# Optimization experiments

Measured on AMD Instinct MI355X. Metric: run time of the kernel, lower is better.

The kernel has to match this reference:

```python
import jax, jax.numpy as jnp
import numpy as np

BN_EPS = 1e-5
CLAMP = 1e-10


def _three_nn(q, p):
    # q: (B,N,3) query points, p: (B,M,3) reference points
    # returns dist (B,N,3) euclidean distance to 3 nearest, idx (B,N,3)
    d2 = (jnp.sum(q * q, -1)[:, :, None] + jnp.sum(p * p, -1)[:, None, :]
          - 2.0 * jnp.einsum('bnd,bmd->bnm', q, p))  # (B,N,M)
    neg_vals, idx = jax.lax.top_k(-d2, 3)
    dist = jnp.sqrt(jnp.maximum(-neg_vals, 1e-20))
    return dist, idx


def _gather(feats_t, idx):
    # feats_t: (B,M,C), idx: (B,N,3) -> (B,N,3,C)
    return jax.vmap(lambda f, i: f[i])(feats_t, idx)


def _conv_bn_relu(x, W, b, g, beta):
    # x: (B,Cin,N); 1x1 Conv1d + BatchNorm1d (training-mode batch stats) + relu
    y = jnp.einsum('oc,bcn->bon', W, x) + b[None, :, None]
    mean = jnp.mean(y, axis=(0, 2), keepdims=True)
    var = jnp.mean((y - mean) ** 2, axis=(0, 2), keepdims=True)
    y = (y - mean) * jax.lax.rsqrt(var + BN_EPS)
    y = y * g[None, :, None] + beta[None, :, None]
    return jax.nn.relu(y)


def setup_inputs() -> dict:
    key = jax.random.key(0)
    ks = jax.random.split(key, 10)
    B, N, M, C2, C1 = 4, 8192, 2048, 256, 128
    inp = {
        'xyz1': jax.random.normal(ks[0], (B, 3, N), jnp.float32),
        'xyz2': jax.random.normal(ks[1], (B, 3, M), jnp.float32),
        'norm1': jax.random.normal(ks[2], (B, 3, N), jnp.float32),
        'norm2': jax.random.normal(ks[3], (B, 3, M), jnp.float32),
        'points1': jax.random.normal(ks[4], (B, C1, N), jnp.float32),
        'points2': jax.random.normal(ks[5], (B, C2, M), jnp.float32),
        'W0': jax.random.normal(ks[6], (256, C2 + C1), jnp.float32) * 0.05,
        'b0': jax.random.normal(ks[7], (256,), jnp.float32) * 0.05,
        'g0': jnp.ones((256,), jnp.float32),
        'be0': jnp.zeros((256,), jnp.float32),
        'W1': jax.random.normal(ks[8], (128, 256), jnp.float32) * 0.05,
        'b1': jax.random.normal(ks[9], (128,), jnp.float32) * 0.05,
        'g1': jnp.ones((128,), jnp.float32),
        'be1': jnp.zeros((128,), jnp.float32),
    }
    return inp


def reference(xyz1, xyz2, norm1, norm2, points1, points2,
              W0, b0, g0, be0, W1, b1, g1, be1):
    B, _, N = xyz1.shape
    # 3-NN search
    dist, idx = _three_nn(jnp.transpose(xyz1, (0, 2, 1)),
                          jnp.transpose(xyz2, (0, 2, 1)))  # (B,N,3)
    # normal distance between query normals and gathered neighbor normals
    grouped_norm = _gather(jnp.transpose(norm2, (0, 2, 1)), idx)        # (B,N,3,3)
    diff = jnp.transpose(norm1, (0, 2, 1))[:, :, None, :] - grouped_norm
    norm_dist = jnp.sqrt(jnp.sum(diff * diff, -1))                       # (B,N,3)
    # distance weights
    recip_dist = 1.0 / jnp.maximum(dist, CLAMP)
    weight = recip_dist / jnp.sum(recip_dist, 2, keepdims=True)
    # normal weights
    recip_nd = 1.0 / jnp.maximum(norm_dist, CLAMP)
    norm_weight = recip_nd / jnp.sum(recip_nd, 2, keepdims=True)
    weight = weight * norm_weight                                        # (B,N,3)
    # three_interpolate: weighted gather of points2
    gathered_pts = _gather(jnp.transpose(points2, (0, 2, 1)), idx)       # (B,N,3,C)
    interpolated = jnp.einsum('bnkc,bnk->bcn', gathered_pts, weight)     # (B,C,N)
    new_points = jnp.concatenate([interpolated, points1], axis=1)        # (B,C+C1,N)
    new_points = _conv_bn_relu(new_points, W0, b0, g0, be0)
    new_points = _conv_bn_relu(new_points, W1, b1, g1, be1)
    return new_points
```

## Files before the change

### kernel.cpp

```cpp
#include <hip/hip_runtime.h>
#include <hip/hip_bf16.h>
#include <cstdint>
#include <cstddef>

static constexpr int BB   = 4;
static constexpr int NN   = 8192;
static constexpr int MM   = 2048;
static constexpr int C1   = 128;
static constexpr int C2   = 256;
static constexpr int CH0  = C2 + C1;
static constexpr int O0   = 256;
static constexpr int O1   = 128;
static constexpr int NCOL = BB * NN;
static constexpr float BN_EPS = 1e-5f;

static constexpr int REC0 = 64;
static constexpr int REC1 = 32;

using u16 = unsigned short;
typedef __attribute__((ext_vector_type(8))) short short8;
typedef __attribute__((ext_vector_type(4))) float f32x4;

static __device__ __forceinline__ float bf2f(u16 u) {
    union { unsigned int i; float f; } v; v.i = ((unsigned int)u) << 16; return v.f;
}
static __device__ __forceinline__ u16 f2bf(float f) {
    union { float f; unsigned int i; } v; v.f = f;
    unsigned int r = (v.i + 0x7fffu + ((v.i >> 16) & 1u)) >> 16;
    return (u16)r;
}

__global__ __launch_bounds__(256) void fused_pre_kernel(
        const float* __restrict__ xyz1,  const float* __restrict__ xyz2,
        const float* __restrict__ norm1, const float* __restrict__ norm2,
        int* __restrict__ idxOut, float* __restrict__ wOut,
        const float* __restrict__ points2, u16* __restrict__ p2T,
        const float* __restrict__ points1, u16* __restrict__ p1T,
        const float* __restrict__ W0f, u16* __restrict__ W0b,
        const float* __restrict__ W1f, u16* __restrict__ W1b,
        float* __restrict__ part0, float* __restrict__ part1) {
#pragma clang fp contract(off)
    __shared__ union { float4 pts[1024]; float tile[32][33]; } sm;
    int id = blockIdx.x;
    int t  = threadIdx.x;

    if (id >= 7680) {
        int flat = (id - 7680) * 256 + t;
        if (flat < 2 * REC0 * 256) part0[flat] = 0.f;
        else part1[flat - 2 * REC0 * 256] = 0.f;
        return;
    }
    if (id >= 1024) {
        int pid = id - 1024;
        if (pid < 6144) {
            const float* in; u16* out; int R, C, b, c0, r0;
            if (pid < 2048) {
                in = points2; out = p2T; R = C2; C = MM;
                b = pid >> 9; int rem = pid & 511;
                c0 = (rem & 63) * 32; r0 = (rem >> 6) * 32;
            } else {
                int id2 = pid - 2048;
                in = points1; out = p1T; R = C1; C = NN;
                b = id2 >> 10; int rem = id2 & 1023;
                c0 = (rem & 255) * 32; r0 = (rem >> 8) * 32;
            }
            int tx = t & 31, ty = t >> 5;
            const float* pin = in + (size_t)b * R * C;
            u16* pout = out + (size_t)b * R * C;
#pragma unroll
            for (int j = 0; j < 4; ++j) {
                int r = ty + j * 8;
                sm.tile[r][tx] = pin[(size_t)(r0 + r) * C + (c0 + tx)];
            }
            __syncthreads();
#pragma unroll
            for (int j = 0; j < 4; ++j) {
                int c = ty + j * 8;
                pout[(size_t)(c0 + c) * R + (r0 + tx)] = f2bf(sm.tile[tx][c]);
            }
        } else {
            int i = (pid - 6144) * 256 + t;
            if (i < O0 * CH0) W0b[i] = f2bf(W0f[i]);
            else {
                int i2 = i - O0 * CH0;
                if (i2 < O1 * O0) W1b[i2] = f2bf(W1f[i2]);
            }
        }
        return;
    }

    int b    = id >> 8;
    int nblk = id & 255;
    int j    = t & 7;

    int n = nblk * 32 + (t >> 3);
    const float* x1 = xyz1 + (size_t)b * 3 * NN;
    float qx = x1[n], qy = x1[NN + n], qz = x1[2 * NN + n];
    float qq = __builtin_fmaf(qx, qx, __builtin_fmaf(qy, qy, qz * qz));

    const float* x2 = xyz2 + (size_t)b * 3 * MM;

    float d0 = 3.4e38f, d1 = 3.4e38f, d2v = 3.4e38f;
    int   i0 = 0, i1 = 0, i2 = 0;

    for (int chunk = 0; chunk < MM / 1024; ++chunk) {
        __syncthreads();
        for (int i = t; i < 1024; i += 256) {
            int m = chunk * 1024 + i;
            float px = x2[m];
            float py = x2[MM + m];
            float pz = x2[2 * MM + m];
            float pp = __builtin_fmaf(px, px, __builtin_fmaf(py, py, pz * pz));
            sm.pts[i] = make_float4(-2.0f * px, -2.0f * py, -2.0f * pz, pp);
        }
        __syncthreads();

#pragma unroll 8
        for (int s = 0; s < 1024 / 8; ++s) {
            int ml = s * 8 + j;
            float4 P = sm.pts[ml];
            float d  = __builtin_fmaf(qx, P.x,
                        __builtin_fmaf(qy, P.y,
                         __builtin_fmaf(qz, P.z, qq + P.w)));
            if (d < d2v) {
                int m = chunk * 1024 + ml;
                if (d < d1) {
                    if (d < d0) { d2v = d1; i2 = i1; d1 = d0; i1 = i0; d0 = d; i0 = m; }
                    else        { d2v = d1; i2 = i1; d1 = d;  i1 = m; }
                } else          { d2v = d;  i2 = m; }
            }
        }
    }

#pragma unroll
    for (int k = 1; k <= 4; k <<= 1) {
        float e0 = __shfl_xor(d0, k, 64), e1 = __shfl_xor(d1, k, 64), e2 = __shfl_xor(d2v, k, 64);
        int   f0 = __shfl_xor(i0, k, 64), f1 = __shfl_xor(i1, k, 64), f2 = __shfl_xor(i2, k, 64);
        float ed[3] = {e0, e1, e2}; int ef[3] = {f0, f1, f2};
#pragma unroll
        for (int e = 0; e < 3; ++e) {
            float dd = ed[e]; int ff = ef[e];
            bool b2 = (dd < d2v) || (dd == d2v && ff < i2);
            if (b2) {
                bool b1 = (dd < d1) || (dd == d1 && ff < i1);
                if (b1) {
                    d2v = d1; i2 = i1;
                    bool b0 = (dd < d0) || (dd == d0 && ff < i0);
                    if (b0) { d1 = d0; i1 = i0; d0 = dd; i0 = ff; }
                    else    { d1 = dd; i1 = ff; }
                } else { d2v = dd; i2 = ff; }
            }
        }
    }

    if (j == 0) {
        float s0 = sqrtf(fmaxf(d0, 1e-20f));
        float s1 = sqrtf(fmaxf(d1, 1e-20f));
        float s2 = sqrtf(fmaxf(d2v, 1e-20f));
        float r0 = 1.0f / fmaxf(s0, 1e-10f);
        float r1 = 1.0f / fmaxf(s1, 1e-10f);
        float r2 = 1.0f / fmaxf(s2, 1e-10f);
        float rs = (r0 + r1) + r2;
        float w0 = r0 / rs, w1 = r1 / rs, w2 = r2 / rs;

        const float* nm1 = norm1 + (size_t)b * 3 * NN;
        const float* nm2 = norm2 + (size_t)b * 3 * MM;
        float ax = nm1[n], ay = nm1[NN + n], az = nm1[2 * NN + n];
        float nd[3]; int ii[3] = {i0, i1, i2};
#pragma unroll
        for (int k = 0; k < 3; ++k) {
            int ik = ii[k];
            float dx = ax - nm2[ik];
            float dy = ay - nm2[MM + ik];
            float dz = az - nm2[2 * MM + ik];
            nd[k] = sqrtf((dx * dx + dy * dy) + dz * dz);
        }
        float m0 = 1.0f / fmaxf(nd[0], 1e-10f);
        float m1 = 1.0f / fmaxf(nd[1], 1e-10f);
        float m2 = 1.0f / fmaxf(nd[2], 1e-10f);
        float ms = (m0 + m1) + m2;

        int col = b * NN + n;
        idxOut[col * 3 + 0] = i0;
        idxOut[col * 3 + 1] = i1;
        idxOut[col * 3 + 2] = i2;
        wOut[col * 3 + 0] = w0 * (m0 / ms);
        wOut[col * 3 + 1] = w1 * (m1 / ms);
        wOut[col * 3 + 2] = w2 * (m2 / ms);
    }
}

template <int KDIM, int LDC, int COLT, int MODE>
__global__ __launch_bounds__(256) void gemm_bt_kernel(const u16* __restrict__ A,
                                                      const u16* __restrict__ Bt,
                                                      const u16* __restrict__ p1T,
                                                      const int* __restrict__ idx,
                                                      const float* __restrict__ w,
                                                      u16* __restrict__ Ct,
                                                      const float* __restrict__ bias,
                                                      const float* __restrict__ redB,
                                                      const float* __restrict__ gB,
                                                      const float* __restrict__ beB,
                                                      float invN,
                                                      float* __restrict__ partials) {
    constexpr int KT  = KDIM / 64;
    constexpr int NI  = COLT / 32;
    constexpr int ASZ = 128 * 64;
    constexpr int BSZ = COLT * 64;
    __shared__ u16 smem[2 * ASZ + 2 * BSZ];
    __shared__ float sSc[MODE == 1 ? KDIM : 1];
    __shared__ float sSh[MODE == 1 ? KDIM : 1];

    int t   = threadIdx.x;
    int l   = t & 63;
    int wv  = t >> 6;
    int rl  = l >> 3;
    int cg  = ((l & 7) ^ rl) * 8;
    int mb0 = blockIdx.y * 128;
    int cb0 = blockIdx.x * COLT;
    int lm  = l & 15;
    int q   = l >> 4;
    int wm0 = (wv & 1) * 64;
    int wn0 = (wv >> 1) * (COLT / 2);

    const u16* Abase = A + (size_t)mb0 * KDIM;

    int vi0 = 0, vi1 = 0, vi2 = 0;
    float vw0 = 0.f, vw1 = 0.f, vw2 = 0.f;
    const u16* p2base = nullptr;
    if (MODE == 2) {
        int colg = cb0 + (t >> 2);
        vi0 = idx[colg * 3 + 0]; vi1 = idx[colg * 3 + 1]; vi2 = idx[colg * 3 + 2];
        vw0 = w[colg * 3 + 0];   vw1 = w[colg * 3 + 1];   vw2 = w[colg * 3 + 2];
        p2base = Bt + (size_t)(cb0 >> 13) * MM * C2;
    }
    if (MODE == 1) {
        int by = t >> 7, chL = t & 127;
        const float* base = redB + (size_t)by * REC0 * 256;
        float s = 0.f, s2 = 0.f;
#pragma unroll 8
        for (int i = 0; i < REC0; ++i) {
            s  += base[i * 256 + chL];
            s2 += base[i * 256 + 128 + chL];
        }
        float mean = s * invN;
        float var  = fmaxf(s2 * invN - mean * mean, 0.f);
        float inv  = rsqrtf(var + BN_EPS);
        float sc   = gB[t] * inv;
        sSc[t] = sc;
        sSh[t] = beB[t] - mean * sc;
        __syncthreads();
    }

    auto stage = [&](int buf, int k0) {
#pragma unroll
        for (int iss = 0; iss < 4; ++iss) {
            int row = wv * 32 + iss * 8;
            const u16* g = Abase + (size_t)(row + rl) * KDIM + k0 + cg;
            __builtin_amdgcn_global_load_lds(
                (const __attribute__((address_space(1))) unsigned int*)g,
                (__attribute__((address_space(3))) unsigned int*)(&smem[buf * ASZ + row * 64]),
                16, 0, 0);
        }
        if (MODE == 1) {
            int row = t >> 2;
            int kc  = (t & 3) * 16;
            const u16* gp = Bt + (size_t)(cb0 + row) * KDIM + k0 + kc;
            union { uint4 v; u16 u[8]; } lo, hi;
            lo.v = *(const uint4*)gp;
            hi.v = *(const uint4*)(gp + 8);
#pragma unroll
            for (int e = 0; e < 8; ++e) {
                float f0 = bf2f(lo.u[e]);
                lo.u[e] = f2bf(fmaxf(f0 * sSc[k0 + kc + e] + sSh[k0 + kc + e], 0.f));
                float f1 = bf2f(hi.u[e]);
                hi.u[e] = f2bf(fmaxf(f1 * sSc[k0 + kc + 8 + e] + sSh[k0 + kc + 8 + e], 0.f));
            }
            int c0 = kc >> 3;
            u16* dstB = &smem[2 * ASZ + buf * BSZ + row * 64];
            *(uint4*)&dstB[((c0)     ^ (row & 7)) * 8] = lo.v;
            *(uint4*)&dstB[((c0 + 1) ^ (row & 7)) * 8] = hi.v;
        } else {
            if (k0 < C2) {
                int row = t >> 2;
                int kc  = (t & 3) * 16;
                const u16* bp = p2base + k0 + kc;
                const u16* r0p = bp + (size_t)vi0 * C2;
                const u16* r1p = bp + (size_t)vi1 * C2;
                const u16* r2p = bp + (size_t)vi2 * C2;
                union { uint4 v; u16 u[8]; } x0, x1, x2, y0, y1, y2, lo, hi;
                x0.v = *(const uint4*)r0p; y0.v = *(const uint4*)(r0p + 8);
                x1.v = *(const uint4*)r1p; y1.v = *(const uint4*)(r1p + 8);
                x2.v = *(const uint4*)r2p; y2.v = *(const uint4*)(r2p + 8);
#pragma unroll
                for (int e = 0; e < 8; ++e) {
                    lo.u[e] = f2bf(vw0 * bf2f(x0.u[e]) + vw1 * bf2f(x1.u[e]) + vw2 * bf2f(x2.u[e]));
                    hi.u[e] = f2bf(vw0 * bf2f(y0.u[e]) + vw1 * bf2f(y1.u[e]) + vw2 * bf2f(y2.u[e]));
                }
                int c0 = kc >> 3;
                u16* dstB = &smem[2 * ASZ + buf * BSZ + row * 64];
                *(uint4*)&dstB[((c0)     ^ (row & 7)) * 8] = lo.v;
                *(uint4*)&dstB[((c0 + 1) ^ (row & 7)) * 8] = hi.v;
            } else {
#pragma unroll
                for (int iss = 0; iss < COLT / 32; ++iss) {
                    int row = wv * (COLT / 4) + iss * 8;
                    const u16* g = p1T + (size_t)(cb0 + row + rl) * C1 + (k0 - C2) + cg;
                    __builtin_amdgcn_global_load_lds(
                        (const __attribute__((address_space(1))) unsigned int*)g,
                        (__attribute__((address_space(3))) unsigned int*)(&smem[2 * ASZ + buf * BSZ + row * 64]),
                        16, 0, 0);
                }
            }
        }
    };

    f32x4 acc[4][NI] = {};

    stage(0, 0);
    for (int kt = 0; kt < KT; ++kt) {
        __syncthreads();
        if (kt + 1 < KT) stage((kt + 1) & 1, (kt + 1) * 64);
        const u16* As = &smem[(kt & 1) * ASZ];
        const u16* Bs = &smem[2 * ASZ + (kt & 1) * BSZ];
#pragma unroll
        for (int ks = 0; ks < 2; ++ks) {
            int csw = ((ks * 4 + q) ^ (lm & 7)) * 8;
            short8 av[4], bv[NI];
#pragma unroll
            for (int mi = 0; mi < 4; ++mi)
                av[mi] = *(const short8*)&As[(wm0 + mi * 16 + lm) * 64 + csw];
#pragma unroll
            for (int ni = 0; ni < NI; ++ni)
                bv[ni] = *(const short8*)&Bs[(wn0 + ni * 16 + lm) * 64 + csw];
#pragma unroll
            for (int mi = 0; mi < 4; ++mi)
#pragma unroll
                for (int ni = 0; ni < NI; ++ni)
                    acc[mi][ni] = __builtin_amdgcn_mfma_f32_16x16x32_bf16(
                        av[mi], bv[ni], acc[mi][ni], 0, 0, 0);
        }
    }

    u16*   Cs   = smem;
    float* reds = (float*)&smem[COLT * 136];

    __syncthreads();
    if (t < 256) reds[t] = 0.f;
    __syncthreads();

#pragma unroll
    for (int mi = 0; mi < 4; ++mi) {
        int chL = wm0 + mi * 16 + q * 4;
        float bv4[4];
#pragma unroll
        for (int r = 0; r < 4; ++r) bv4[r] = bias[mb0 + chL + r];
        float s[4]  = {0.f, 0.f, 0.f, 0.f};
        float s2[4] = {0.f, 0.f, 0.f, 0.f};
#pragma unroll
        for (int ni = 0; ni < NI; ++ni) {
            int colL = wn0 + ni * 16 + lm;
            union { u16 u[4]; uint2 d; } pk;
#pragma unroll
            for (int r = 0; r < 4; ++r) {
                float v = acc[mi][ni][r] + bv4[r];
                s[r]  += v;
                s2[r] += v * v;
                pk.u[r] = f2bf(v);
            }
            *(uint2*)&Cs[colL * 136 + chL] = pk.d;
        }
#pragma unroll
        for (int r = 0; r < 4; ++r) {
            float a = s[r], b2 = s2[r];
#pragma unroll
            for (int off = 1; off < 16; off <<= 1) {
                a  += __shfl_xor(a, off, 64);
                b2 += __shfl_xor(b2, off, 64);
            }
            if (lm == 0) {
                atomicAdd(&reds[chL + r], a);
                atomicAdd(&reds[128 + chL + r], b2);
            }
        }
    }
    __syncthreads();

    for (int u = t; u < COLT * 2; u += 256) {
        int c = u >> 1, h = u & 1;
        const u16* src = &Cs[c * 136 + h * 64];
        u16* dst = Ct + (size_t)(cb0 + c) * LDC + mb0 + h * 64;
#pragma unroll
        for (int jj = 0; jj < 8; ++jj)
            *(uint4*)(dst + jj * 8) = *(const uint4*)(src + jj * 8);
    }
    int recIdx = (MODE == 2) ? (blockIdx.y * REC0 + (blockIdx.x & (REC0 - 1)))
                             : (blockIdx.x & (REC1 - 1));
    atomicAdd(&partials[(size_t)recIdx * 256 + t], reds[t]);
}

__global__ __launch_bounds__(256) void finalize_kernel(const u16* __restrict__ y1T,
                                                       const float* __restrict__ part1,
                                                       const float* __restrict__ g1,
                                                       const float* __restrict__ be1,
                                                       float invN,
                                                       float* __restrict__ out) {
    __shared__ float tile[64][129];
    __shared__ float sc[O1], sh[O1];
    int t  = threadIdx.x;
    int b  = blockIdx.y;
    int n0 = blockIdx.x * 64;

    if (t < O1) {
        float s = 0.f, s2 = 0.f;
#pragma unroll 8
        for (int i = 0; i < REC1; ++i) {
            s  += part1[i * 256 + t];
            s2 += part1[i * 256 + 128 + t];
        }
        float mean = s * invN;
        float var  = fmaxf(s2 * invN - mean * mean, 0.f);
        float inv  = rsqrtf(var + BN_EPS);
        float scv  = g1[t] * inv;
        sc[t] = scv;
        sh[t] = be1[t] - mean * scv;
    }
    __syncthreads();

#pragma unroll
    for (int it = 0; it < 32; ++it) {
        int flat = it * 256 + t;
        int cl = flat >> 7;
        int c  = flat & 127;
        int col = b * NN + n0 + cl;
        float v = bf2f(y1T[(size_t)col * O1 + c]);
        tile[cl][c] = fmaxf(v * sc[c] + sh[c], 0.f);
    }
    __syncthreads();
#pragma unroll
    for (int it = 0; it < 32; ++it) {
        int flat = it * 256 + t;
        int c  = flat >> 6;
        int nl = flat & 63;
        out[(size_t)b * O1 * NN + (size_t)c * NN + n0 + nl] = tile[nl][c];
    }
}

extern "C" void kernel_launch(void* const* d_in, const int* in_sizes, int n_in,
                              void* d_out, int out_size, void* d_ws, size_t ws_size,
                              hipStream_t stream) {
    (void)in_sizes; (void)n_in; (void)out_size; (void)ws_size;

    const float* xyz1    = (const float*)d_in[0];
    const float* xyz2    = (const float*)d_in[1];
    const float* norm1   = (const float*)d_in[2];
    const float* norm2   = (const float*)d_in[3];
    const float* points1 = (const float*)d_in[4];
    const float* points2 = (const float*)d_in[5];
    const float* W0f     = (const float*)d_in[6];
    const float* b0      = (const float*)d_in[7];
    const float* g0      = (const float*)d_in[8];
    const float* be0     = (const float*)d_in[9];
    const float* W1f     = (const float*)d_in[10];
    const float* b1      = (const float*)d_in[11];
    const float* g1      = (const float*)d_in[12];
    const float* be1     = (const float*)d_in[13];
    float* out = (float*)d_out;

    char* w8 = (char*)d_ws;
    size_t off = 0;
    auto carve = [&](size_t bytes) { void* p = w8 + off; off += (bytes + 255) & ~(size_t)255; return p; };
    int*   idxW   = (int*)  carve((size_t)NCOL * 3 * sizeof(int));
    float* wW     = (float*)carve((size_t)NCOL * 3 * sizeof(float));
    u16*   p2T    = (u16*)  carve((size_t)BB * MM * C2 * 2);
    u16*   p1T    = (u16*)  carve((size_t)BB * NN * C1 * 2);
    u16*   W0b    = (u16*)  carve((size_t)O0 * CH0 * 2);
    u16*   W1b    = (u16*)  carve((size_t)O1 * O0 * 2);
    u16*   y0T    = (u16*)  carve((size_t)NCOL * O0 * 2);
    u16*   y1T    = (u16*)  carve((size_t)NCOL * O1 * 2);
    float* part0  = (float*)carve((size_t)2 * REC0 * 256 * sizeof(float));
    float* part1  = (float*)carve((size_t)REC1 * 256 * sizeof(float));

    const float invN = 1.0f / (float)NCOL;

    fused_pre_kernel<<<7840, 256, 0, stream>>>(
        xyz1, xyz2, norm1, norm2, idxW, wW,
        points2, p2T, points1, p1T, W0f, W0b, W1f, W1b, part0, part1);

    gemm_bt_kernel<CH0, O0, 64, 2><<<dim3(NCOL / 64, O0 / 128), 256, 0, stream>>>(
        W0b, p2T, p1T, idxW, wW, y0T, b0, nullptr, nullptr, nullptr, invN, part0);

    gemm_bt_kernel<O0, O1, 64, 1><<<dim3(NCOL / 64, O1 / 128), 256, 0, stream>>>(
        W1b, y0T, nullptr, nullptr, nullptr, y1T, b1, part0, g0, be0, invN, part1);

    finalize_kernel<<<dim3(NN / 64, BB), 256, 0, stream>>>(y1T, part1, g1, be1, invN, out);
}
```

Before: 182.8 us.

## Fuse second GEMM with BN finalize using a cooperative grid sync

The second 1x1-conv GEMM and the final BatchNorm+ReLU+transpose kernel are merged into one cooperative kernel. Each block keeps its bf16 output tile in shared memory, adds its partial statistics, waits at a grid-wide barrier, then normalises and writes the transposed fp32 output directly. This removes the y1T intermediate write and read and one kernel launch. In exchange it requires all 512 blocks to be co-resident and adds the cost of a grid-wide barrier.

```diff
diff --git a/kernel.cpp b/kernel.cpp
--- a/kernel.cpp
+++ b/kernel.cpp
@@ -1,7 +1,10 @@
 #include <hip/hip_runtime.h>
 #include <hip/hip_bf16.h>
+#include <hip/hip_cooperative_groups.h>
 #include <cstdint>
 #include <cstddef>
+
+namespace cg = cooperative_groups;
 
 static constexpr int BB   = 4;
 static constexpr int NN   = 8192;
@@ -215,7 +218,7 @@
     int l   = t & 63;
     int wv  = t >> 6;
     int rl  = l >> 3;
-    int cg  = ((l & 7) ^ rl) * 8;
+    int cg_ = ((l & 7) ^ rl) * 8;
     int mb0 = blockIdx.y * 128;
     int cb0 = blockIdx.x * COLT;
     int lm  = l & 15;
@@ -256,7 +259,7 @@
 #pragma unroll
         for (int iss = 0; iss < 4; ++iss) {
             int row = wv * 32 + iss * 8;
-            const u16* g = Abase + (size_t)(row + rl) * KDIM + k0 + cg;
+            const u16* g = Abase + (size_t)(row + rl) * KDIM + k0 + cg_;
             __builtin_amdgcn_global_load_lds(
                 (const __attribute__((address_space(1))) unsigned int*)g,
                 (__attribute__((address_space(3))) unsigned int*)(&smem[buf * ASZ + row * 64]),
@@ -305,7 +308,7 @@
 #pragma unroll
                 for (int iss = 0; iss < COLT / 32; ++iss) {
                     int row = wv * (COLT / 4) + iss * 8;
-                    const u16* g = p1T + (size_t)(cb0 + row + rl) * C1 + (k0 - C2) + cg;
+                    const u16* g = p1T + (size_t)(cb0 + row + rl) * C1 + (k0 - C2) + cg_;
                     __builtin_amdgcn_global_load_lds(
                         (const __attribute__((address_space(1))) unsigned int*)g,
                         (__attribute__((address_space(3))) unsigned int*)(&smem[2 * ASZ + buf * BSZ + row * 64]),
@@ -399,50 +402,191 @@
     atomicAdd(&partials[(size_t)recIdx * 256 + t], reds[t]);
 }
 
-__global__ __launch_bounds__(256) void finalize_kernel(const u16* __restrict__ y1T,
-                                                       const float* __restrict__ part1,
-                                                       const float* __restrict__ g1,
-                                                       const float* __restrict__ be1,
-                                                       float invN,
-                                                       float* __restrict__ out) {
-    __shared__ float tile[64][129];
-    __shared__ float sc[O1], sh[O1];
-    int t  = threadIdx.x;
-    int b  = blockIdx.y;
-    int n0 = blockIdx.x * 64;
+__global__ __launch_bounds__(256) void gemm1_final_kernel(
+        const u16* __restrict__ A,
+        const u16* __restrict__ Bt,
+        const float* __restrict__ bias,
+        const float* __restrict__ redB,
+        const float* __restrict__ gB,
+        const float* __restrict__ beB,
+        float invN,
+        float* __restrict__ partials,
+        const float* __restrict__ g1,
+        const float* __restrict__ be1,
+        float* __restrict__ out) {
+    constexpr int KDIM = O0;
+    constexpr int COLT = 64;
+    constexpr int KT  = KDIM / 64;
+    constexpr int NI  = COLT / 32;
+    constexpr int ASZ = 128 * 64;
+    constexpr int BSZ = COLT * 64;
+    __shared__ u16 smem[2 * ASZ + 2 * BSZ];
+    __shared__ float sSc[KDIM];
+    __shared__ float sSh[KDIM];
+
+    int t   = threadIdx.x;
+    int l   = t & 63;
+    int wv  = t >> 6;
+    int rl  = l >> 3;
+    int cg_ = ((l & 7) ^ rl) * 8;
+    int cb0 = blockIdx.x * COLT;
+    int lm  = l & 15;
+    int q   = l >> 4;
+    int wm0 = (wv & 1) * 64;
+    int wn0 = (wv >> 1) * (COLT / 2);
+
+    const u16* Abase = A;
+
+    {
+        int by = t >> 7, chL = t & 127;
+        const float* base = redB + (size_t)by * REC0 * 256;
+        float s = 0.f, s2 = 0.f;
+#pragma unroll 8
+        for (int i = 0; i < REC0; ++i) {
+            s  += base[i * 256 + chL];
+            s2 += base[i * 256 + 128 + chL];
+        }
+        float mean = s * invN;
+        float var  = fmaxf(s2 * invN - mean * mean, 0.f);
+        float inv  = rsqrtf(var + BN_EPS);
+        float sc   = gB[t] * inv;
+        sSc[t] = sc;
+        sSh[t] = beB[t] - mean * sc;
+        __syncthreads();
+    }
+
+    auto stage = [&](int buf, int k0) {
+#pragma unroll
+        for (int iss = 0; iss < 4; ++iss) {
+            int row = wv * 32 + iss * 8;
+            const u16* g = Abase + (size_t)(row + rl) * KDIM + k0 + cg_;
+            __builtin_amdgcn_global_load_lds(
+                (const __attribute__((address_space(1))) unsigned int*)g,
+                (__attribute__((address_space(3))) unsigned int*)(&smem[buf * ASZ + row * 64]),
+                16, 0, 0);
+        }
+        {
+            int row = t >> 2;
+            int kc  = (t & 3) * 16;
+            const u16* gp = Bt + (size_t)(cb0 + row) * KDIM + k0 + kc;
+            union { uint4 v; u16 u[8]; } lo, hi;
+            lo.v = *(const uint4*)gp;
+            hi.v = *(const uint4*)(gp + 8);
+#pragma unroll
+            for (int e = 0; e < 8; ++e) {
+                float f0 = bf2f(lo.u[e]);
+                lo.u[e] = f2bf(fmaxf(f0 * sSc[k0 + kc + e] + sSh[k0 + kc + e], 0.f));
+                float f1 = bf2f(hi.u[e]);
+                hi.u[e] = f2bf(fmaxf(f1 * sSc[k0 + kc + 8 + e] + sSh[k0 + kc + 8 + e], 0.f));
+            }
+            int c0 = kc >> 3;
+            u16* dstB = &smem[2 * ASZ + buf * BSZ + row * 64];
+            *(uint4*)&dstB[((c0)     ^ (row & 7)) * 8] = lo.v;
+            *(uint4*)&dstB[((c0 + 1) ^ (row & 7)) * 8] = hi.v;
+        }
+    };
+
+    f32x4 acc[4][NI] = {};
+
+    stage(0, 0);
+    for (int kt = 0; kt < KT; ++kt) {
+        __syncthreads();
+        if (kt + 1 < KT) stage((kt + 1) & 1, (kt + 1) * 64);
+        const u16* As = &smem[(kt & 1) * ASZ];
+        const u16* Bs = &smem[2 * ASZ + (kt & 1) * BSZ];
+#pragma unroll
+        for (int ks = 0; ks < 2; ++ks) {
+            int csw = ((ks * 4 + q) ^ (lm & 7)) * 8;
+            short8 av[4], bv[NI];
+#pragma unroll
+            for (int mi = 0; mi < 4; ++mi)
+                av[mi] = *(const short8*)&As[(wm0 + mi * 16 + lm) * 64 + csw];
+#pragma unroll
+            for (int ni = 0; ni < NI; ++ni)
+                bv[ni] = *(const short8*)&Bs[(wn0 + ni * 16 + lm) * 64 + csw];
+#pragma unroll
+            for (int mi = 0; mi < 4; ++mi)
+#pragma unroll
+                for (int ni = 0; ni < NI; ++ni)
+                    acc[mi][ni] = __builtin_amdgcn_mfma_f32_16x16x32_bf16(
+                        av[mi], bv[ni], acc[mi][ni], 0, 0, 0);
+        }
+    }
+
+    u16*   Cs   = smem;
+    float* reds = (float*)&smem[COLT * 136];
+
+    __syncthreads();
+    if (t < 256) reds[t] = 0.f;
+    __syncthreads();
+
+#pragma unroll
+    for (int mi = 0; mi < 4; ++mi) {
+        int chL = wm0 + mi * 16 + q * 4;
+        float bv4[4];
+#pragma unroll
+        for (int r = 0; r < 4; ++r) bv4[r] = bias[chL + r];
+        float s[4]  = {0.f, 0.f, 0.f, 0.f};
+        float s2[4] = {0.f, 0.f, 0.f, 0.f};
+#pragma unroll
+        for (int ni = 0; ni < NI; ++ni) {
+            int colL = wn0 + ni * 16 + lm;
+            union { u16 u[4]; uint2 d; } pk;
+#pragma unroll
+            for (int r = 0; r < 4; ++r) {
+                float v = acc[mi][ni][r] + bv4[r];
+                s[r]  += v;
+                s2[r] += v * v;
+                pk.u[r] = f2bf(v);
+            }
+            *(uint2*)&Cs[colL * 136 + chL] = pk.d;
+        }
+#pragma unroll
+        for (int r = 0; r < 4; ++r) {
+            float a = s[r], b2 = s2[r];
+#pragma unroll
+            for (int off = 1; off < 16; off <<= 1) {
+                a  += __shfl_xor(a, off, 64);
+                b2 += __shfl_xor(b2, off, 64);
+            }
+            if (lm == 0) {
+                atomicAdd(&reds[chL + r], a);
+                atomicAdd(&reds[128 + chL + r], b2);
+            }
+        }
+    }
+    __syncthreads();
+
+    int recIdx = blockIdx.x & (REC1 - 1);
+    atomicAdd(&partials[(size_t)recIdx * 256 + t], reds[t]);
+
+    cg::this_grid().sync();
 
     if (t < O1) {
         float s = 0.f, s2 = 0.f;
 #pragma unroll 8
         for (int i = 0; i < REC1; ++i) {
-            s  += part1[i * 256 + t];
-            s2 += part1[i * 256 + 128 + t];
+            s  += partials[i * 256 + t];
+            s2 += partials[i * 256 + 128 + t];
         }
         float mean = s * invN;
         float var  = fmaxf(s2 * invN - mean * mean, 0.f);
         float inv  = rsqrtf(var + BN_EPS);
         float scv  = g1[t] * inv;
-        sc[t] = scv;
-        sh[t] = be1[t] - mean * scv;
+        sSc[t] = scv;
+        sSh[t] = be1[t] - mean * scv;
     }
     __syncthreads();
 
-#pragma unroll
-    for (int it = 0; it < 32; ++it) {
-        int flat = it * 256 + t;
-        int cl = flat >> 7;
-        int c  = flat & 127;
-        int col = b * NN + n0 + cl;
-        float v = bf2f(y1T[(size_t)col * O1 + c]);
-        tile[cl][c] = fmaxf(v * sc[c] + sh[c], 0.f);
-    }
-    __syncthreads();
-#pragma unroll
-    for (int it = 0; it < 32; ++it) {
-        int flat = it * 256 + t;
-        int c  = flat >> 6;
-        int nl = flat & 63;
-        out[(size_t)b * O1 * NN + (size_t)c * NN + n0 + nl] = tile[nl][c];
+    int bb = cb0 >> 13;
+    int n0 = cb0 & (NN - 1);
+    float* obase = out + (size_t)bb * O1 * NN + n0;
+#pragma unroll
+    for (int iter = 0; iter < 32; ++iter) {
+        int c    = (t >> 6) + 4 * iter;
+        int colL = t & 63;
+        float v = bf2f(Cs[colL * 136 + c]);
+        obase[(size_t)c * NN + colL] = fmaxf(v * sSc[c] + sSh[c], 0.f);
     }
 }
 
@@ -477,7 +621,6 @@
     u16*   W0b    = (u16*)  carve((size_t)O0 * CH0 * 2);
     u16*   W1b    = (u16*)  carve((size_t)O1 * O0 * 2);
     u16*   y0T    = (u16*)  carve((size_t)NCOL * O0 * 2);
-    u16*   y1T    = (u16*)  carve((size_t)NCOL * O1 * 2);
     float* part0  = (float*)carve((size_t)2 * REC0 * 256 * sizeof(float));
     float* part1  = (float*)carve((size_t)REC1 * 256 * sizeof(float));
 
@@ -490,8 +633,16 @@
     gemm_bt_kernel<CH0, O0, 64, 2><<<dim3(NCOL / 64, O0 / 128), 256, 0, stream>>>(
         W0b, p2T, p1T, idxW, wW, y0T, b0, nullptr, nullptr, nullptr, invN, part0);
 
-    gemm_bt_kernel<O0, O1, 64, 1><<<dim3(NCOL / 64, O1 / 128), 256, 0, stream>>>(
-        W1b, y0T, nullptr, nullptr, nullptr, y1T, b1, part0, g0, be0, invN, part1);
-
-    finalize_kernel<<<dim3(NN / 64, BB), 256, 0, stream>>>(y1T, part1, g1, be1, invN, out);
+    {
+        const u16* A  = W1b;
+        const u16* Bt = y0T;
+        void* args[] = {
+            (void*)&A, (void*)&Bt, (void*)&b1,
+            (void*)&part0, (void*)&g0, (void*)&be0,
+            (void*)&invN, (void*)&part1,
+            (void*)&g1, (void*)&be1, (void*)&out
+        };
+        hipLaunchCooperativeKernel((void*)gemm1_final_kernel,
+                                   dim3(NCOL / 64), dim3(256), args, 0, stream);
+    }
 }
```

New measurement: 252.9 us. 38.3% more time.

## Compute all 256 output channels per block in first GEMM to avoid duplicate gathers

Applied to the files above, without the earlier changes.

The first GEMM previously ran two blocks per column tile, one for each 128-channel half, so every block repeated the three-NN weighted gather of points2 and the points1 load. The new dedicated kernel computes all 256 output rows per block with a 256x64 tile and 8x2 MFMA accumulators. The gather and interpolation now happen once per column tile. This costs more registers and LDS per block (launch bounds of 2 blocks per CU) and the grid is half as large. The statistics partial layout and the second GEMM's reduction are updated to match.

```diff
diff --git a/kernel.cpp b/kernel.cpp
--- a/kernel.cpp
+++ b/kernel.cpp
@@ -46,8 +46,8 @@
 
     if (id >= 7680) {
         int flat = (id - 7680) * 256 + t;
-        if (flat < 2 * REC0 * 256) part0[flat] = 0.f;
-        else part1[flat - 2 * REC0 * 256] = 0.f;
+        if (flat < REC0 * 512) part0[flat] = 0.f;
+        else part1[flat - REC0 * 512] = 0.f;
         return;
     }
     if (id >= 1024) {
@@ -190,58 +190,204 @@
     }
 }
 
-template <int KDIM, int LDC, int COLT, int MODE>
-__global__ __launch_bounds__(256) void gemm_bt_kernel(const u16* __restrict__ A,
-                                                      const u16* __restrict__ Bt,
-                                                      const u16* __restrict__ p1T,
-                                                      const int* __restrict__ idx,
-                                                      const float* __restrict__ w,
-                                                      u16* __restrict__ Ct,
-                                                      const float* __restrict__ bias,
-                                                      const float* __restrict__ redB,
-                                                      const float* __restrict__ gB,
-                                                      const float* __restrict__ beB,
-                                                      float invN,
-                                                      float* __restrict__ partials) {
+__global__ __launch_bounds__(256, 2) void gemm0_kernel(
+        const u16* __restrict__ A,
+        const u16* __restrict__ Bt,
+        const u16* __restrict__ p1T,
+        const int* __restrict__ idx,
+        const float* __restrict__ w,
+        u16* __restrict__ Ct,
+        const float* __restrict__ bias,
+        float* __restrict__ partials) {
+    constexpr int KDIM = CH0;
+    constexpr int COLT = 64;
+    constexpr int KT  = KDIM / 64;
+    constexpr int NI  = COLT / 32;
+    constexpr int ASZ = 256 * 64;
+    constexpr int BSZ = COLT * 64;
+    __shared__ u16 smem[2 * ASZ + 2 * BSZ];
+
+    int t   = threadIdx.x;
+    int l   = t & 63;
+    int wv  = t >> 6;
+    int rl  = l >> 3;
+    int cg_ = ((l & 7) ^ rl) * 8;
+    int cb0 = blockIdx.x * COLT;
+    int lm  = l & 15;
+    int q   = l >> 4;
+    int wm0 = (wv & 1) * 64;
+    int wn0 = (wv >> 1) * (COLT / 2);
+
+    int colg = cb0 + (t >> 2);
+    int vi0 = idx[colg * 3 + 0], vi1 = idx[colg * 3 + 1], vi2 = idx[colg * 3 + 2];
+    float vw0 = w[colg * 3 + 0], vw1 = w[colg * 3 + 1], vw2 = w[colg * 3 + 2];
+    const u16* p2base = Bt + (size_t)(cb0 >> 13) * MM * C2;
+
+    auto stage = [&](int buf, int k0) {
+#pragma unroll
+        for (int iss = 0; iss < 8; ++iss) {
+            int row = wv * 64 + iss * 8;
+            const u16* g = A + (size_t)(row + rl) * KDIM + k0 + cg_;
+            __builtin_amdgcn_global_load_lds(
+                (const __attribute__((address_space(1))) unsigned int*)g,
+                (__attribute__((address_space(3))) unsigned int*)(&smem[buf * ASZ + row * 64]),
+                16, 0, 0);
+        }
+        if (k0 < C2) {
+            int row = t >> 2;
+            int kc  = (t & 3) * 16;
+            const u16* bp = p2base + k0 + kc;
+            const u16* r0p = bp + (size_t)vi0 * C2;
+            const u16* r1p = bp + (size_t)vi1 * C2;
+            const u16* r2p = bp + (size_t)vi2 * C2;
+            union { uint4 v; u16 u[8]; } x0, x1, x2, y0, y1, y2, lo, hi;
+            x0.v = *(const uint4*)r0p; y0.v = *(const uint4*)(r0p + 8);
+            x1.v = *(const uint4*)r1p; y1.v = *(const uint4*)(r1p + 8);
+            x2.v = *(const uint4*)r2p; y2.v = *(const uint4*)(r2p + 8);
+#pragma unroll
+            for (int e = 0; e < 8; ++e) {
+                lo.u[e] = f2bf(vw0 * bf2f(x0.u[e]) + vw1 * bf2f(x1.u[e]) + vw2 * bf2f(x2.u[e]));
+                hi.u[e] = f2bf(vw0 * bf2f(y0.u[e]) + vw1 * bf2f(y1.u[e]) + vw2 * bf2f(y2.u[e]));
+            }
+            int c0 = kc >> 3;
+            u16* dstB = &smem[2 * ASZ + buf * BSZ + row * 64];
+            *(uint4*)&dstB[((c0)     ^ (row & 7)) * 8] = lo.v;
+            *(uint4*)&dstB[((c0 + 1) ^ (row & 7)) * 8] = hi.v;
+        } else {
+#pragma unroll
+            for (int iss = 0; iss < 2; ++iss) {
+                int row = wv * 16 + iss * 8;
+                const u16* g = p1T + (size_t)(cb0 + row + rl) * C1 + (k0 - C2) + cg_;
+                __builtin_amdgcn_global_load_lds(
+                    (const __attribute__((address_space(1))) unsigned int*)g,
+                    (__attribute__((address_space(3))) unsigned int*)(&smem[2 * ASZ + buf * BSZ + row * 64]),
+                    16, 0, 0);
+            }
+        }
+    };
+
+    f32x4 acc[8][NI] = {};
+
+    stage(0, 0);
+    for (int kt = 0; kt < KT; ++kt) {
+        __syncthreads();
+        if (kt + 1 < KT) stage((kt + 1) & 1, (kt + 1) * 64);
+        const u16* As = &smem[(kt & 1) * ASZ];
+        const u16* Bs = &smem[2 * ASZ + (kt & 1) * BSZ];
+#pragma unroll
+        for (int ks = 0; ks < 2; ++ks) {
+            int csw = ((ks * 4 + q) ^ (lm & 7)) * 8;
+            short8 av[8], bv[NI];
+#pragma unroll
+            for (int mi = 0; mi < 8; ++mi) {
+                int mrow = (mi >> 2) * 128 + wm0 + (mi & 3) * 16;
+                av[mi] = *(const short8*)&As[(mrow + lm) * 64 + csw];
+            }
+#pragma unroll
+            for (int ni = 0; ni < NI; ++ni)
+                bv[ni] = *(const short8*)&Bs[(wn0 + ni * 16 + lm) * 64 + csw];
+#pragma unroll
+            for (int mi = 0; mi < 8; ++mi)
+#pragma unroll
+                for (int ni = 0; ni < NI; ++ni)
+                    acc[mi][ni] = __builtin_amdgcn_mfma_f32_16x16x32_bf16(
+                        av[mi], bv[ni], acc[mi][ni], 0, 0, 0);
+        }
+    }
+
+    u16*   Cs   = smem;
+    float* reds = (float*)&smem[COLT * 264];
+
+    __syncthreads();
+    reds[t] = 0.f; reds[256 + t] = 0.f;
+    __syncthreads();
+
+#pragma unroll
+    for (int mi = 0; mi < 8; ++mi) {
+        int chL = (mi >> 2) * 128 + wm0 + (mi & 3) * 16 + q * 4;
+        float bv4[4];
+#pragma unroll
+        for (int r = 0; r < 4; ++r) bv4[r] = bias[chL + r];
+        float s[4]  = {0.f, 0.f, 0.f, 0.f};
+        float s2[4] = {0.f, 0.f, 0.f, 0.f};
+#pragma unroll
+        for (int ni = 0; ni < NI; ++ni) {
+            int colL = wn0 + ni * 16 + lm;
+            union { u16 u[4]; uint2 d; } pk;
+#pragma unroll
+            for (int r = 0; r < 4; ++r) {
+                float v = acc[mi][ni][r] + bv4[r];
+                s[r]  += v;
+                s2[r] += v * v;
+                pk.u[r] = f2bf(v);
+            }
+            *(uint2*)&Cs[colL * 264 + chL] = pk.d;
+        }
+#pragma unroll
+        for (int r = 0; r < 4; ++r) {
+            float a = s[r], b2 = s2[r];
+#pragma unroll
+            for (int off = 1; off < 16; off <<= 1) {
+                a  += __shfl_xor(a, off, 64);
+                b2 += __shfl_xor(b2, off, 64);
+            }
+            if (lm == 0) {
+                atomicAdd(&reds[chL + r], a);
+                atomicAdd(&reds[256 + chL + r], b2);
+            }
+        }
+    }
+    __syncthreads();
+
+    {
+        int c = t >> 2, h = t & 3;
+        const u16* src = &Cs[c * 264 + h * 64];
+        u16* dst = Ct + (size_t)(cb0 + c) * O0 + h * 64;
+#pragma unroll
+        for (int jj = 0; jj < 8; ++jj)
+            *(uint4*)(dst + jj * 8) = *(const uint4*)(src + jj * 8);
+    }
+    int recIdx = blockIdx.x & (REC0 - 1);
+    atomicAdd(&partials[(size_t)recIdx * 512 + t], reds[t]);
+    atomicAdd(&partials[(size_t)recIdx * 512 + 256 + t], reds[256 + t]);
+}
+
+__global__ __launch_bounds__(256) void gemm1_kernel(const u16* __restrict__ A,
+                                                    const u16* __restrict__ Bt,
+                                                    u16* __restrict__ Ct,
+                                                    const float* __restrict__ bias,
+                                                    const float* __restrict__ redB,
+                                                    const float* __restrict__ gB,
+                                                    const float* __restrict__ beB,
+                                                    float invN,
+                                                    float* __restrict__ partials) {
+    constexpr int KDIM = O0;
+    constexpr int COLT = 64;
     constexpr int KT  = KDIM / 64;
     constexpr int NI  = COLT / 32;
     constexpr int ASZ = 128 * 64;
     constexpr int BSZ = COLT * 64;
     __shared__ u16 smem[2 * ASZ + 2 * BSZ];
-    __shared__ float sSc[MODE == 1 ? KDIM : 1];
-    __shared__ float sSh[MODE == 1 ? KDIM : 1];
+    __shared__ float sSc[KDIM];
+    __shared__ float sSh[KDIM];
 
     int t   = threadIdx.x;
     int l   = t & 63;
     int wv  = t >> 6;
     int rl  = l >> 3;
-    int cg  = ((l & 7) ^ rl) * 8;
-    int mb0 = blockIdx.y * 128;
+    int cg_ = ((l & 7) ^ rl) * 8;
     int cb0 = blockIdx.x * COLT;
     int lm  = l & 15;
     int q   = l >> 4;
     int wm0 = (wv & 1) * 64;
     int wn0 = (wv >> 1) * (COLT / 2);
 
-    const u16* Abase = A + (size_t)mb0 * KDIM;
-
-    int vi0 = 0, vi1 = 0, vi2 = 0;
-    float vw0 = 0.f, vw1 = 0.f, vw2 = 0.f;
-    const u16* p2base = nullptr;
-    if (MODE == 2) {
-        int colg = cb0 + (t >> 2);
-        vi0 = idx[colg * 3 + 0]; vi1 = idx[colg * 3 + 1]; vi2 = idx[colg * 3 + 2];
-        vw0 = w[colg * 3 + 0];   vw1 = w[colg * 3 + 1];   vw2 = w[colg * 3 + 2];
-        p2base = Bt + (size_t)(cb0 >> 13) * MM * C2;
-    }
-    if (MODE == 1) {
-        int by = t >> 7, chL = t & 127;
-        const float* base = redB + (size_t)by * REC0 * 256;
+    {
         float s = 0.f, s2 = 0.f;
 #pragma unroll 8
         for (int i = 0; i < REC0; ++i) {
-            s  += base[i * 256 + chL];
-            s2 += base[i * 256 + 128 + chL];
+            s  += redB[i * 512 + t];
+            s2 += redB[i * 512 + 256 + t];
         }
         float mean = s * invN;
         float var  = fmaxf(s2 * invN - mean * mean, 0.f);
@@ -256,13 +402,13 @@
 #pragma unroll
         for (int iss = 0; iss < 4; ++iss) {
             int row = wv * 32 + iss * 8;
-            const u16* g = Abase + (size_t)(row + rl) * KDIM + k0 + cg;
+            const u16* g = A + (size_t)(row + rl) * KDIM + k0 + cg_;
             __builtin_amdgcn_global_load_lds(
                 (const __attribute__((address_space(1))) unsigned int*)g,
                 (__attribute__((address_space(3))) unsigned int*)(&smem[buf * ASZ + row * 64]),
                 16, 0, 0);
         }
-        if (MODE == 1) {
+        {
             int row = t >> 2;
             int kc  = (t & 3) * 16;
             const u16* gp = Bt + (size_t)(cb0 + row) * KDIM + k0 + kc;
@@ -280,38 +426,6 @@
             u16* dstB = &smem[2 * ASZ + buf * BSZ + row * 64];
             *(uint4*)&dstB[((c0)     ^ (row & 7)) * 8] = lo.v;
             *(uint4*)&dstB[((c0 + 1) ^ (row & 7)) * 8] = hi.v;
-        } else {
-            if (k0 < C2) {
-                int row = t >> 2;
-                int kc  = (t & 3) * 16;
-                const u16* bp = p2base + k0 + kc;
-                const u16* r0p = bp + (size_t)vi0 * C2;
-                const u16* r1p = bp + (size_t)vi1 * C2;
-                const u16* r2p = bp + (size_t)vi2 * C2;
-                union { uint4 v; u16 u[8]; } x0, x1, x2, y0, y1, y2, lo, hi;
-                x0.v = *(const uint4*)r0p; y0.v = *(const uint4*)(r0p + 8);
-                x1.v = *(const uint4*)r1p; y1.v = *(const uint4*)(r1p + 8);
-                x2.v = *(const uint4*)r2p; y2.v = *(const uint4*)(r2p + 8);
-#pragma unroll
-                for (int e = 0; e < 8; ++e) {
-                    lo.u[e] = f2bf(vw0 * bf2f(x0.u[e]) + vw1 * bf2f(x1.u[e]) + vw2 * bf2f(x2.u[e]));
-                    hi.u[e] = f2bf(vw0 * bf2f(y0.u[e]) + vw1 * bf2f(y1.u[e]) + vw2 * bf2f(y2.u[e]));
-                }
-                int c0 = kc >> 3;
-                u16* dstB = &smem[2 * ASZ + buf * BSZ + row * 64];
-                *(uint4*)&dstB[((c0)     ^ (row & 7)) * 8] = lo.v;
-                *(uint4*)&dstB[((c0 + 1) ^ (row & 7)) * 8] = hi.v;
-            } else {
-#pragma unroll
-                for (int iss = 0; iss < COLT / 32; ++iss) {
-                    int row = wv * (COLT / 4) + iss * 8;
-                    const u16* g = p1T + (size_t)(cb0 + row + rl) * C1 + (k0 - C2) + cg;
-                    __builtin_amdgcn_global_load_lds(
-                        (const __attribute__((address_space(1))) unsigned int*)g,
-                        (__attribute__((address_space(3))) unsigned int*)(&smem[2 * ASZ + buf * BSZ + row * 64]),
-                        16, 0, 0);
-                }
-            }
         }
     };
 
@@ -354,7 +468,7 @@
         int chL = wm0 + mi * 16 + q * 4;
         float bv4[4];
 #pragma unroll
-        for (int r = 0; r < 4; ++r) bv4[r] = bias[mb0 + chL + r];
+        for (int r = 0; r < 4; ++r) bv4[r] = bias[chL + r];
         float s[4]  = {0.f, 0.f, 0.f, 0.f};
         float s2[4] = {0.f, 0.f, 0.f, 0.f};
 #pragma unroll
@@ -389,13 +503,12 @@
     for (int u = t; u < COLT * 2; u += 256) {
         int c = u >> 1, h = u & 1;
         const u16* src = &Cs[c * 136 + h * 64];
-        u16* dst = Ct + (size_t)(cb0 + c) * LDC + mb0 + h * 64;
+        u16* dst = Ct + (size_t)(cb0 + c) * O1 + h * 64;
 #pragma unroll
         for (int jj = 0; jj < 8; ++jj)
             *(uint4*)(dst + jj * 8) = *(const uint4*)(src + jj * 8);
     }
-    int recIdx = (MODE == 2) ? (blockIdx.y * REC0 + (blockIdx.x & (REC0 - 1)))
-                             : (blockIdx.x & (REC1 - 1));
+    int recIdx = blockIdx.x & (REC1 - 1);
     atomicAdd(&partials[(size_t)recIdx * 256 + t], reds[t]);
 }
 
@@ -478,7 +591,7 @@
     u16*   W1b    = (u16*)  carve((size_t)O1 * O0 * 2);
     u16*   y0T    = (u16*)  carve((size_t)NCOL * O0 * 2);
     u16*   y1T    = (u16*)  carve((size_t)NCOL * O1 * 2);
-    float* part0  = (float*)carve((size_t)2 * REC0 * 256 * sizeof(float));
+    float* part0  = (float*)carve((size_t)REC0 * 512 * sizeof(float));
     float* part1  = (float*)carve((size_t)REC1 * 256 * sizeof(float));
 
     const float invN = 1.0f / (float)NCOL;
@@ -487,11 +600,11 @@
         xyz1, xyz2, norm1, norm2, idxW, wW,
         points2, p2T, points1, p1T, W0f, W0b, W1f, W1b, part0, part1);
 
-    gemm_bt_kernel<CH0, O0, 64, 2><<<dim3(NCOL / 64, O0 / 128), 256, 0, stream>>>(
-        W0b, p2T, p1T, idxW, wW, y0T, b0, nullptr, nullptr, nullptr, invN, part0);
-
-    gemm_bt_kernel<O0, O1, 64, 1><<<dim3(NCOL / 64, O1 / 128), 256, 0, stream>>>(
-        W1b, y0T, nullptr, nullptr, nullptr, y1T, b1, part0, g0, be0, invN, part1);
+    gemm0_kernel<<<NCOL / 64, 256, 0, stream>>>(
+        W0b, p2T, p1T, idxW, wW, y0T, b0, part0);
+
+    gemm1_kernel<<<NCOL / 64, 256, 0, stream>>>(
+        W1b, y0T, y1T, b1, part0, g0, be0, invN, part1);
 
     finalize_kernel<<<dim3(NN / 64, BB), 256, 0, stream>>>(y1T, part1, g1, be1, invN, out);
 }
```

Measured after the change: 180.8 us. Within noise of the previous version (-1.1%).
